# Kernel tuning notes

Measured on AMD Instinct MI355X. Metric: run time of the kernel, lower is better.

Reference implementation:

```python
import jax, jax.numpy as jnp
import numpy as np

B_, S_, D_, N_, R_ = 2, 2048, 1024, 16, 64  # batch, seq, d_model, d_state, dt_rank


def setup_inputs() -> dict:
    key = jax.random.key(0)
    ks = jax.random.split(key, 12)
    x = jax.random.normal(ks[0], (B_, S_, D_), dtype=jnp.float32)
    # params (xavier-ish scale)
    W_dtw = jax.random.normal(ks[1], (R_, D_), dtype=jnp.float32) * (1.0 / np.sqrt(D_))
    W_dt = jax.random.normal(ks[2], (D_, R_), dtype=jnp.float32) * (1.0 / np.sqrt(R_))
    b_dt = jnp.zeros((D_,), dtype=jnp.float32)
    A_log = jnp.log(jax.random.uniform(ks[3], (D_, N_), minval=0.5, maxval=1.5, dtype=jnp.float32))
    W_B = jax.random.normal(ks[4], (N_, D_), dtype=jnp.float32) * (1.0 / np.sqrt(D_))
    W_C = jax.random.normal(ks[5], (N_, D_), dtype=jnp.float32) * (1.0 / np.sqrt(D_))
    Dp = jnp.ones((D_,), dtype=jnp.float32)
    ln_g = jnp.ones((D_,), dtype=jnp.float32)
    ln_b = jnp.zeros((D_,), dtype=jnp.float32)
    W_out = jax.random.normal(ks[6], (D_, D_), dtype=jnp.float32) * (1.0 / np.sqrt(D_))
    return {"x": x, "W_dtw": W_dtw, "W_dt": W_dt, "b_dt": b_dt, "A_log": A_log,
            "W_B": W_B, "W_C": W_C, "Dp": Dp, "ln_g": ln_g, "ln_b": ln_b, "W_out": W_out}


def _layernorm(y, g, b, eps=1e-5):
    mu = jnp.mean(y, axis=-1, keepdims=True)
    var = jnp.mean(jnp.square(y - mu), axis=-1, keepdims=True)
    return (y - mu) * jax.lax.rsqrt(var + eps) * g + b


def reference(x, W_dtw, W_dt, b_dt, A_log, W_B, W_C, Dp, ln_g, ln_b, W_out):
    # projections
    dt = jnp.einsum('bsd,rd->bsr', x, W_dtw)                 # [B,S,R]
    delta = jax.nn.softplus(jnp.einsum('bsr,dr->bsd', dt, W_dt) + b_dt)  # [B,S,D]
    Bm = jnp.einsum('bsd,nd->bsn', x, W_B)                   # [B,S,N]
    Cm = jnp.einsum('bsd,nd->bsn', x, W_C)                   # [B,S,N]
    A = -jnp.exp(A_log)                                      # [D,N]

    def step(h, inp):
        d_t, b_t, c_t, x_t = inp                             # [B,D],[B,N],[B,N],[B,D]
        dA = jnp.exp(d_t[..., None] * A)                     # [B,D,N]
        h = dA * h + (d_t[..., None] * b_t[:, None, :]) * x_t[..., None]
        y_t = jnp.sum(h * c_t[:, None, :], axis=-1)          # [B,D]
        return h, y_t

    h0 = jnp.zeros((x.shape[0], x.shape[2], A.shape[1]), dtype=x.dtype)
    xs = (jnp.swapaxes(delta, 0, 1), jnp.swapaxes(Bm, 0, 1),
          jnp.swapaxes(Cm, 0, 1), jnp.swapaxes(x, 0, 1))
    _, ys = jax.lax.scan(step, h0, xs)                       # ys: [S,B,D]
    y = jnp.swapaxes(ys, 0, 1) + Dp * x                      # [B,S,D]
    y = _layernorm(y, ln_g, ln_b)
    return jnp.einsum('bsd,ed->bse', y, W_out)
```

## Files before the change

kernel.cpp:

```cpp
#include <hip/hip_runtime.h>
#include <hip/hip_bf16.h>

#define B_ 2
#define S_ 2048
#define D_ 1024
#define N_ 16
#define R_ 64
#define NC 64
#define CL 32
#define BS_ (B_*S_)
#define KSPLIT 8

typedef __attribute__((ext_vector_type(4))) float f32x4;
typedef __attribute__((ext_vector_type(8))) short bf16x8;
typedef __attribute__((ext_vector_type(8))) unsigned short u16x8;

__device__ __forceinline__ unsigned short f2b(float v) {
  unsigned u = __builtin_bit_cast(unsigned, v);
  unsigned r = ((u >> 16) & 1u) + 0x7FFFu;
  return (unsigned short)((u + r) >> 16);
}

__device__ __forceinline__ void gload_lds16(const void* g, void* l) {
  __builtin_amdgcn_global_load_lds(
      (const __attribute__((address_space(1))) unsigned int*)g,
      (__attribute__((address_space(3))) unsigned int*)l, 16, 0, 0);
}

__global__ __launch_bounds__(256) void k_castall(
    const float* __restrict__ W_dtw, const float* __restrict__ W_B,
    const float* __restrict__ W_C, const float* __restrict__ W_dt,
    const float* __restrict__ W_out,
    unsigned short* __restrict__ Wcat, unsigned short* __restrict__ wdtb,
    unsigned short* __restrict__ wob) {
  int i = (blockIdx.x * 256 + threadIdx.x) * 4;
  const float* s; unsigned short* d; int off;
  if (i < 65536)       { s = W_dtw; d = Wcat;         off = 0; }
  else if (i < 81920)  { s = W_B;   d = Wcat + 65536; off = 65536; }
  else if (i < 98304)  { s = W_C;   d = Wcat + 81920; off = 81920; }
  else if (i < 163840) { s = W_dt;  d = wdtb;         off = 98304; }
  else                 { s = W_out; d = wob;          off = 163840; }
  int j = i - off;
  float4 v = *(const float4*)&s[j];
  ushort4 o;
  o.x = f2b(v.x); o.y = f2b(v.y); o.z = f2b(v.z); o.w = f2b(v.w);
  *(ushort4*)&d[j] = o;
}

__global__ __launch_bounds__(256, 2) void k_proj(
    const float* __restrict__ x, const unsigned short* __restrict__ Wcat,
    float* __restrict__ part) {
  __shared__ __align__(16) unsigned short Xs[2][64 * 64];
  __shared__ __align__(16) unsigned short Ws[2][96 * 64];
  const int tid = threadIdx.x;
  const int lane = tid & 63, w = tid >> 6;
  const size_t row0 = (size_t)blockIdx.x * 64;
  const int kbase = blockIdx.y * (D_ / KSPLIT);
  f32x4 acc[6] = {};

  auto stage = [&](int buf, int k0) {
    #pragma unroll
    for (int i = 0; i < 2; ++i) {
      int id = i * 256 + tid; int row = id >> 3, s = id & 7;
      const float* gp = &x[(row0 + row) * D_ + k0 + s * 8];
      float4 v0 = *(const float4*)gp;
      float4 v1 = *(const float4*)(gp + 4);
      u16x8 u;
      u[0] = f2b(v0.x); u[1] = f2b(v0.y); u[2] = f2b(v0.z); u[3] = f2b(v0.w);
      u[4] = f2b(v1.x); u[5] = f2b(v1.y); u[6] = f2b(v1.z); u[7] = f2b(v1.w);
      *(u16x8*)&Xs[buf][row * 64 + ((s ^ (row & 7)) << 3)] = u;
    }
    #pragma unroll
    for (int i = 0; i < 3; ++i) {
      int id = i * 256 + tid; int row = id >> 3, s = id & 7;
      gload_lds16(Wcat + (size_t)row * D_ + k0 + ((s ^ (row & 7)) << 3),
                  Ws[buf] + row * 64 + s * 8);
    }
  };
  stage(0, kbase);
  __syncthreads();
  int cur = 0;
  const int r = lane & 15, kg = lane >> 4;
  for (int t = 0; t < 2; ++t) {
    if (t < 1) stage(cur ^ 1, kbase + 64);
    #pragma unroll
    for (int ks = 0; ks < 2; ++ks) {
      const int arow = w * 16 + r;
      bf16x8 a = *(const bf16x8*)&Xs[cur][arow * 64 + ((((ks << 2) | kg) ^ (arow & 7)) << 3)];
      #pragma unroll
      for (int nt = 0; nt < 6; ++nt) {
        const int brow = nt * 16 + r;
        bf16x8 b = *(const bf16x8*)&Ws[cur][brow * 64 + ((((ks << 2) | kg) ^ (brow & 7)) << 3)];
        acc[nt] = __builtin_amdgcn_mfma_f32_16x16x32_bf16(a, b, acc[nt], 0, 0, 0);
      }
    }
    __syncthreads();
    cur ^= 1;
  }
  const int cr = lane >> 4, cc = lane & 15;
  float* pb = part + (size_t)blockIdx.y * (BS_ * 96);
  #pragma unroll
  for (int nt = 0; nt < 6; ++nt)
    #pragma unroll
    for (int j = 0; j < 4; ++j)
      pb[(row0 + w * 16 + cr * 4 + j) * 96 + nt * 16 + cc] = acc[nt][j];
}

__global__ __launch_bounds__(256) void k_projred(
    const float* __restrict__ part, unsigned short* __restrict__ dtb,
    float* __restrict__ Bm, float* __restrict__ Cm) {
  int e = blockIdx.x * 256 + threadIdx.x;
  int row = e / 96, col = e - row * 96;
  float s = 0.f;
  #pragma unroll
  for (int p = 0; p < KSPLIT; ++p) s += part[e + (size_t)p * (BS_ * 96)];
  if (col < 64)      dtb[row * R_ + col] = f2b(s);
  else if (col < 80) Bm[row * N_ + col - 64] = s;
  else               Cm[row * N_ + col - 80] = s;
}

__global__ __launch_bounds__(256) void k_delta(
    const unsigned short* __restrict__ dtb, const unsigned short* __restrict__ wdtb,
    const float* __restrict__ b_dt, float* __restrict__ delta) {
  __shared__ __align__(16) unsigned short As[128 * 64];
  __shared__ __align__(16) unsigned short Bs[128 * 64];
  const int tid = threadIdx.x;
  const int lane = tid & 63, wid = tid >> 6;
  const int wr = wid >> 1, wc = wid & 1;
  const size_t row0 = (size_t)blockIdx.x * 128;
  const size_t col0 = (size_t)blockIdx.y * 128;
  f32x4 acc[4][4] = {};

  {
    const int r = tid >> 3, s = tid & 7;
    #pragma unroll
    for (int i = 0; i < 4; ++i) {
      const int row = i * 32 + r;
      const int gs = s ^ (row & 7);
      gload_lds16(dtb + (row0 + row) * R_ + gs * 8, As + row * 64 + s * 8);
      gload_lds16(wdtb + (col0 + row) * R_ + gs * 8, Bs + row * 64 + s * 8);
    }
  }
  __syncthreads();
  const int r = lane & 15, kg = lane >> 4;
  #pragma unroll
  for (int ks = 0; ks < 2; ++ks) {
    bf16x8 a[4], b[4];
    #pragma unroll
    for (int m = 0; m < 4; ++m) {
      const int arow = wr * 64 + m * 16 + r;
      a[m] = *(const bf16x8*)&As[arow * 64 + (((ks << 2) | kg) ^ (arow & 7)) * 8];
    }
    #pragma unroll
    for (int n = 0; n < 4; ++n) {
      const int brow = wc * 64 + n * 16 + r;
      b[n] = *(const bf16x8*)&Bs[brow * 64 + (((ks << 2) | kg) ^ (brow & 7)) * 8];
    }
    #pragma unroll
    for (int m = 0; m < 4; ++m)
      #pragma unroll
      for (int n = 0; n < 4; ++n)
        acc[m][n] = __builtin_amdgcn_mfma_f32_16x16x32_bf16(a[m], b[n], acc[m][n], 0, 0, 0);
  }
  const int cr = lane >> 4, cc = lane & 15;
  #pragma unroll
  for (int m = 0; m < 4; ++m) {
    #pragma unroll
    for (int n = 0; n < 4; ++n) {
      const int d = (int)col0 + wc * 64 + n * 16 + cc;
      const float bd = b_dt[d];
      #pragma unroll
      for (int j = 0; j < 4; ++j) {
        size_t trow = row0 + wr * 64 + m * 16 + cr * 4 + j;
        float v = acc[m][n][j] + bd;
        float sp = fmaxf(v, 0.f) + log1pf(__expf(-fabsf(v)));
        delta[trow * D_ + d] = sp;
      }
    }
  }
}

__global__ __launch_bounds__(256) void k_scan1(
    const float* __restrict__ x, const float* __restrict__ delta,
    const float* __restrict__ Bm, const float* __restrict__ A_log,
    float* __restrict__ aprod, float* __restrict__ hend) {
  __shared__ __align__(16) float sd[CL][64];
  __shared__ __align__(16) float sx[CL][64];
  __shared__ __align__(16) float sB[CL][N_];
  const int tid = threadIdx.x;
  const int db = blockIdx.x & 15;
  const int c  = (blockIdx.x >> 4) & (NC - 1);
  const int b  = blockIdx.x >> 10;
  const int d0 = db * 64;
  const size_t tokbase = (size_t)(b * S_ + c * CL);

  {
    int s = tid >> 4, jf = (tid & 15) * 4;
    size_t g = (tokbase + s) * D_ + d0 + jf;
    gload_lds16(&delta[g], &sd[s][jf]);
    gload_lds16(&x[g],     &sx[s][jf]);
    gload_lds16(&delta[g + (size_t)16 * D_], &sd[s + 16][jf]);
    gload_lds16(&x[g + (size_t)16 * D_],     &sx[s + 16][jf]);
    if (tid < 128) {
      int s2 = tid >> 2, nf = (tid & 3) * 4;
      gload_lds16(&Bm[(tokbase + s2) * N_ + nf], &sB[s2][nf]);
    }
  }
  const int nq = tid & 3, dl = tid >> 2;
  const int d = d0 + dl;
  float4 av = *(const float4*)&A_log[(size_t)d * N_ + nq * 4];
  float Ad0 = -__expf(av.x), Ad1 = -__expf(av.y);
  float Ad2 = -__expf(av.z), Ad3 = -__expf(av.w);
  __syncthreads();

  float ap0 = 1.f, ap1 = 1.f, ap2 = 1.f, ap3 = 1.f;
  float h0 = 0.f, h1 = 0.f, h2 = 0.f, h3 = 0.f;
  #pragma unroll 8
  for (int s = 0; s < CL; ++s) {
    float dlt = sd[s][dl];
    float dbx = dlt * sx[s][dl];
    float4 Bv = *(const float4*)&sB[s][nq * 4];
    float da0 = __expf(dlt * Ad0), da1 = __expf(dlt * Ad1);
    float da2 = __expf(dlt * Ad2), da3 = __expf(dlt * Ad3);
    ap0 *= da0; ap1 *= da1; ap2 *= da2; ap3 *= da3;
    h0 = da0 * h0 + dbx * Bv.x;
    h1 = da1 * h1 + dbx * Bv.y;
    h2 = da2 * h2 + dbx * Bv.z;
    h3 = da3 * h3 + dbx * Bv.w;
  }
  size_t o = (((size_t)(b * NC + c)) * D_ + d) * N_ + nq * 4;
  *(float4*)&aprod[o] = make_float4(ap0, ap1, ap2, ap3);
  *(float4*)&hend[o]  = make_float4(h0, h1, h2, h3);
}

__global__ __launch_bounds__(256) void k_scan2(
    const float* __restrict__ aprod, const float* __restrict__ hend,
    float* __restrict__ hstart) {
  int g = blockIdx.x * 256 + threadIdx.x;
  int n = g & (N_ - 1);
  int d = (g >> 4) & (D_ - 1);
  int b = g >> 14;
  float h = 0.f;
  for (int c = 0; c < NC; ++c) {
    size_t idx = (((size_t)b * NC + c) * D_ + d) * N_ + n;
    hstart[idx] = h;
    h = aprod[idx] * h + hend[idx];
  }
}

__global__ __launch_bounds__(256) void k_scan3(
    const float* __restrict__ x, const float* __restrict__ delta,
    const float* __restrict__ Bm, const float* __restrict__ Cm,
    const float* __restrict__ A_log, const float* __restrict__ hstart,
    const float* __restrict__ Dp, float* __restrict__ ypre) {
  __shared__ __align__(16) float sd[CL][64];
  __shared__ __align__(16) float sx[CL][64];
  __shared__ __align__(16) float sB[CL][N_];
  __shared__ __align__(16) float sC[CL][N_];
  __shared__ __align__(16) float sy[CL][64];
  const int tid = threadIdx.x;
  const int db = blockIdx.x & 15;
  const int c  = (blockIdx.x >> 4) & (NC - 1);
  const int b  = blockIdx.x >> 10;
  const int d0 = db * 64;
  const size_t tokbase = (size_t)(b * S_ + c * CL);

  {
    int s = tid >> 4, jf = (tid & 15) * 4;
    size_t g = (tokbase + s) * D_ + d0 + jf;
    gload_lds16(&delta[g], &sd[s][jf]);
    gload_lds16(&x[g],     &sx[s][jf]);
    gload_lds16(&delta[g + (size_t)16 * D_], &sd[s + 16][jf]);
    gload_lds16(&x[g + (size_t)16 * D_],     &sx[s + 16][jf]);
    if (tid < 128) {
      int s2 = tid >> 2, nf = (tid & 3) * 4;
      gload_lds16(&Bm[(tokbase + s2) * N_ + nf], &sB[s2][nf]);
      gload_lds16(&Cm[(tokbase + s2) * N_ + nf], &sC[s2][nf]);
    }
  }
  const int nq = tid & 3, dl = tid >> 2;
  const int d = d0 + dl;
  float4 av = *(const float4*)&A_log[(size_t)d * N_ + nq * 4];
  float Ad0 = -__expf(av.x), Ad1 = -__expf(av.y);
  float Ad2 = -__expf(av.z), Ad3 = -__expf(av.w);
  float h0, h1, h2, h3;
  {
    size_t o = (((size_t)(b * NC + c)) * D_ + d) * N_ + nq * 4;
    float4 v = *(const float4*)&hstart[o];
    h0 = v.x; h1 = v.y; h2 = v.z; h3 = v.w;
  }
  const float Dpd = Dp[d];
  __syncthreads();

  #pragma unroll 8
  for (int s = 0; s < CL; ++s) {
    float dlt = sd[s][dl];
    float xv  = sx[s][dl];
    float dbx = dlt * xv;
    float4 Bv = *(const float4*)&sB[s][nq * 4];
    float4 Cv = *(const float4*)&sC[s][nq * 4];
    float da0 = __expf(dlt * Ad0), da1 = __expf(dlt * Ad1);
    float da2 = __expf(dlt * Ad2), da3 = __expf(dlt * Ad3);
    h0 = da0 * h0 + dbx * Bv.x;
    h1 = da1 * h1 + dbx * Bv.y;
    h2 = da2 * h2 + dbx * Bv.z;
    h3 = da3 * h3 + dbx * Bv.w;
    float y = h0 * Cv.x + h1 * Cv.y + h2 * Cv.z + h3 * Cv.w;
    y += __shfl_xor(y, 1);
    y += __shfl_xor(y, 2);
    if (nq == 0) sy[s][dl] = y + Dpd * xv;
  }
  __syncthreads();
  {
    int s = tid >> 3, j = (tid & 7) * 8;
    size_t g = (tokbase + s) * D_ + d0 + j;
    *(float4*)&ypre[g]     = *(float4*)&sy[s][j];
    *(float4*)&ypre[g + 4] = *(float4*)&sy[s][j + 4];
  }
}

__device__ __forceinline__ float block_sum256(float v, float* sm) {
  #pragma unroll
  for (int o = 32; o > 0; o >>= 1) v += __shfl_down(v, o, 64);
  int w = threadIdx.x >> 6;
  __syncthreads();
  if ((threadIdx.x & 63) == 0) sm[w] = v;
  __syncthreads();
  return (sm[0] + sm[1]) + (sm[2] + sm[3]);
}

__global__ __launch_bounds__(256) void k_ln(
    const float* __restrict__ ypre, const float* __restrict__ g,
    const float* __restrict__ bta, unsigned short* __restrict__ ybf) {
  __shared__ float sm[4];
  const int t = blockIdx.x;
  const int tid = threadIdx.x;
  size_t base = (size_t)t * D_ + tid * 4;
  float4 v = *(const float4*)&ypre[base];
  float s1 = block_sum256(v.x + v.y + v.z + v.w, sm);
  float mu = s1 * (1.f / D_);
  float cx = v.x - mu, cy = v.y - mu, cz = v.z - mu, cw = v.w - mu;
  float s2 = block_sum256(cx*cx + cy*cy + cz*cz + cw*cw, sm);
  float rs = rsqrtf(s2 * (1.f / D_) + 1e-5f);
  float4 gg = *(const float4*)&g[tid * 4];
  float4 bb = *(const float4*)&bta[tid * 4];
  ushort4 o;
  o.x = f2b(cx * rs * gg.x + bb.x);
  o.y = f2b(cy * rs * gg.y + bb.y);
  o.z = f2b(cz * rs * gg.z + bb.z);
  o.w = f2b(cw * rs * gg.w + bb.w);
  *(ushort4*)&ybf[base] = o;
}

__device__ __forceinline__ void stage128x64(const unsigned short* __restrict__ g,
                                            size_t row0, int k0,
                                            unsigned short* lds, int tid) {
  const int r = tid >> 3, s = tid & 7;
  #pragma unroll
  for (int i = 0; i < 4; ++i) {
    const int row = i * 32 + r;
    const int gs = s ^ (row & 7);
    gload_lds16(g + ((row0 + row) << 10) + k0 + (gs << 3), lds + row * 64 + s * 8);
  }
}

__device__ __forceinline__ void stage64x64(const unsigned short* __restrict__ g,
                                           size_t row0, int k0,
                                           unsigned short* lds, int tid) {
  const int r = tid >> 3, s = tid & 7;
  #pragma unroll
  for (int i = 0; i < 2; ++i) {
    const int row = i * 32 + r;
    const int gs = s ^ (row & 7);
    gload_lds16(g + ((row0 + row) << 10) + k0 + (gs << 3), lds + row * 64 + s * 8);
  }
}

__global__ __launch_bounds__(256, 2) void k_out(const unsigned short* __restrict__ Y,
                                                const unsigned short* __restrict__ W,
                                                float* __restrict__ O) {
  __shared__ __align__(16) unsigned short As[2][128 * 64];
  __shared__ __align__(16) unsigned short Bs[2][64 * 64];
  const int tid = threadIdx.x;
  const int lane = tid & 63, wid = tid >> 6;
  const size_t row0 = (size_t)blockIdx.x * 128;
  const size_t col0 = (size_t)blockIdx.y * 64;
  f32x4 acc[2][4] = {};

  stage128x64(Y, row0, 0, As[0], tid);
  stage64x64(W, col0, 0, Bs[0], tid);
  __syncthreads();

  int cur = 0;
  const int r = lane & 15, kg = lane >> 4;
  for (int t = 0; t < 16; ++t) {
    if (t + 1 < 16) {
      stage128x64(Y, row0, (t + 1) * 64, As[cur ^ 1], tid);
      stage64x64(W, col0, (t + 1) * 64, Bs[cur ^ 1], tid);
    }
    #pragma unroll
    for (int ks = 0; ks < 2; ++ks) {
      bf16x8 a[2], b[4];
      #pragma unroll
      for (int m = 0; m < 2; ++m) {
        const int arow = wid * 32 + m * 16 + r;
        a[m] = *(const bf16x8*)&As[cur][arow * 64 + (((ks << 2) | kg) ^ (arow & 7)) * 8];
      }
      #pragma unroll
      for (int n = 0; n < 4; ++n) {
        const int brow = n * 16 + r;
        b[n] = *(const bf16x8*)&Bs[cur][brow * 64 + (((ks << 2) | kg) ^ (brow & 7)) * 8];
      }
      #pragma unroll
      for (int m = 0; m < 2; ++m)
        #pragma unroll
        for (int n = 0; n < 4; ++n)
          acc[m][n] = __builtin_amdgcn_mfma_f32_16x16x32_bf16(a[m], b[n], acc[m][n], 0, 0, 0);
    }
    __syncthreads();
    cur ^= 1;
  }

  const int cr = lane >> 4, cc = lane & 15;
  #pragma unroll
  for (int m = 0; m < 2; ++m) {
    #pragma unroll
    for (int n = 0; n < 4; ++n) {
      size_t orow = row0 + wid * 32 + m * 16 + cr * 4;
      float* op = O + orow * D_ + col0 + n * 16 + cc;
      #pragma unroll
      for (int j = 0; j < 4; ++j) op[(size_t)j * D_] = acc[m][n][j];
    }
  }
}

extern "C" void kernel_launch(void* const* d_in, const int* in_sizes, int n_in,
                              void* d_out, int out_size, void* d_ws, size_t ws_size,
                              hipStream_t stream) {
  const float* x     = (const float*)d_in[0];
  const float* W_dtw = (const float*)d_in[1];
  const float* W_dt  = (const float*)d_in[2];
  const float* b_dt  = (const float*)d_in[3];
  const float* A_log = (const float*)d_in[4];
  const float* W_B   = (const float*)d_in[5];
  const float* W_C   = (const float*)d_in[6];
  const float* Dp    = (const float*)d_in[7];
  const float* ln_g  = (const float*)d_in[8];
  const float* ln_b  = (const float*)d_in[9];
  const float* W_out = (const float*)d_in[10];
  float* out = (float*)d_out;

  float* ws = (float*)d_ws;
  float* delta  = ws;
  float* ypre   = delta  + (size_t)BS_ * D_;
  float* Bm     = ypre   + (size_t)BS_ * D_;
  float* Cm     = Bm     + (size_t)BS_ * N_;
  float* aprod  = Cm     + (size_t)BS_ * N_;
  float* hend   = aprod  + (size_t)B_ * NC * D_ * N_;
  float* hstart = hend   + (size_t)B_ * NC * D_ * N_;
  float* part   = hstart + (size_t)B_ * NC * D_ * N_;
  unsigned short* Wcat = (unsigned short*)(part + (size_t)KSPLIT * BS_ * 96);
  unsigned short* wdtb = Wcat + (size_t)96 * D_;
  unsigned short* wob  = wdtb + (size_t)D_ * R_;
  unsigned short* ybf  = wob  + (size_t)D_ * D_;
  unsigned short* dtb  = ybf  + (size_t)BS_ * D_;

  k_castall<<<dim3(1184), dim3(256), 0, stream>>>(W_dtw, W_B, W_C, W_dt, W_out,
                                                  Wcat, wdtb, wob);
  k_proj<<<dim3(BS_ / 64, KSPLIT), dim3(256), 0, stream>>>(x, Wcat, part);
  k_projred<<<dim3(BS_ * 96 / 256), dim3(256), 0, stream>>>(part, dtb, Bm, Cm);
  k_delta<<<dim3(BS_ / 128, D_ / 128), dim3(256), 0, stream>>>(dtb, wdtb, b_dt, delta);
  k_scan1<<<dim3(B_ * NC * (D_ / 64)), dim3(256), 0, stream>>>(x, delta, Bm, A_log,
                                                               aprod, hend);
  k_scan2<<<dim3(B_ * D_ * N_ / 256), dim3(256), 0, stream>>>(aprod, hend, hstart);
  k_scan3<<<dim3(B_ * NC * (D_ / 64)), dim3(256), 0, stream>>>(x, delta, Bm, Cm,
                                                               A_log, hstart, Dp, ypre);
  k_ln<<<dim3(BS_), dim3(256), 0, stream>>>(ypre, ln_g, ln_b, ybf);
  k_out<<<dim3(BS_ / 128, D_ / 64), dim3(256), 0, stream>>>(ybf, wob, out);
}
```

Baseline: 110.6 us.

## Replace per-state chunk decay products with delta sums and parallelize inter-chunk scan

The chunk scan now stores one per-channel sum of delta instead of a per-state product of decays, and the inter-chunk pass rebuilds each decay as exp(A*sum). The second pass splits the 64 chunks across 8 lanes, combining them with a shuffle-based prefix, so the sequential chain drops from 64 dependent steps to about 23. Separately, the output GEMM tile shrinks from 128x64 to 64x64 with higher occupancy, giving more blocks at the cost of less data reuse per block.

```diff
diff --git a/kernel.cpp b/kernel.cpp
--- a/kernel.cpp
+++ b/kernel.cpp
@@ -183,7 +183,7 @@
 __global__ __launch_bounds__(256) void k_scan1(
     const float* __restrict__ x, const float* __restrict__ delta,
     const float* __restrict__ Bm, const float* __restrict__ A_log,
-    float* __restrict__ aprod, float* __restrict__ hend) {
+    float* __restrict__ sdsum, float* __restrict__ hend) {
   __shared__ __align__(16) float sd[CL][64];
   __shared__ __align__(16) float sx[CL][64];
   __shared__ __align__(16) float sB[CL][N_];
@@ -213,38 +213,63 @@
   float Ad2 = -__expf(av.z), Ad3 = -__expf(av.w);
   __syncthreads();
 
-  float ap0 = 1.f, ap1 = 1.f, ap2 = 1.f, ap3 = 1.f;
+  float sds = 0.f;
   float h0 = 0.f, h1 = 0.f, h2 = 0.f, h3 = 0.f;
   #pragma unroll 8
   for (int s = 0; s < CL; ++s) {
     float dlt = sd[s][dl];
     float dbx = dlt * sx[s][dl];
+    sds += dlt;
     float4 Bv = *(const float4*)&sB[s][nq * 4];
     float da0 = __expf(dlt * Ad0), da1 = __expf(dlt * Ad1);
     float da2 = __expf(dlt * Ad2), da3 = __expf(dlt * Ad3);
-    ap0 *= da0; ap1 *= da1; ap2 *= da2; ap3 *= da3;
     h0 = da0 * h0 + dbx * Bv.x;
     h1 = da1 * h1 + dbx * Bv.y;
     h2 = da2 * h2 + dbx * Bv.z;
     h3 = da3 * h3 + dbx * Bv.w;
   }
   size_t o = (((size_t)(b * NC + c)) * D_ + d) * N_ + nq * 4;
-  *(float4*)&aprod[o] = make_float4(ap0, ap1, ap2, ap3);
-  *(float4*)&hend[o]  = make_float4(h0, h1, h2, h3);
+  *(float4*)&hend[o] = make_float4(h0, h1, h2, h3);
+  if (nq == 0) sdsum[(size_t)(b * NC + c) * D_ + d] = sds;
 }
 
 __global__ __launch_bounds__(256) void k_scan2(
-    const float* __restrict__ aprod, const float* __restrict__ hend,
-    float* __restrict__ hstart) {
-  int g = blockIdx.x * 256 + threadIdx.x;
-  int n = g & (N_ - 1);
-  int d = (g >> 4) & (D_ - 1);
-  int b = g >> 14;
+    const float* __restrict__ sdsum, const float* __restrict__ hend,
+    const float* __restrict__ A_log, float* __restrict__ hstart) {
+  const int tid = threadIdx.x;
+  const int o  = tid & 7;
+  const int n  = (tid >> 3) & 15;
+  const int dl = tid >> 7;
+  const int d2 = blockIdx.x & 511;
+  const int b  = blockIdx.x >> 9;
+  const int d  = d2 * 2 + dl;
+  const float Ad = -__expf(A_log[(size_t)d * N_ + n]);
+
+  float ap8[8], he8[8];
+  float A_loc = 1.f, H_loc = 0.f;
+  #pragma unroll
+  for (int k = 0; k < 8; ++k) {
+    const int c = o * 8 + k;
+    float sds = sdsum[(size_t)(b * NC + c) * D_ + d];
+    float ap = __expf(Ad * sds);
+    float he = hend[((size_t)(b * NC + c) * D_ + d) * N_ + n];
+    ap8[k] = ap; he8[k] = he;
+    A_loc *= ap;
+    H_loc = ap * H_loc + he;
+  }
   float h = 0.f;
-  for (int c = 0; c < NC; ++c) {
-    size_t idx = (((size_t)b * NC + c) * D_ + d) * N_ + n;
-    hstart[idx] = h;
-    h = aprod[idx] * h + hend[idx];
+  const int gb = (tid & 63) & ~7;
+  #pragma unroll
+  for (int j = 0; j < 7; ++j) {
+    float Aj = __shfl(A_loc, gb | j, 64);
+    float Hj = __shfl(H_loc, gb | j, 64);
+    if (o > j) h = Aj * h + Hj;
+  }
+  #pragma unroll
+  for (int k = 0; k < 8; ++k) {
+    const int c = o * 8 + k;
+    hstart[((size_t)(b * NC + c) * D_ + d) * N_ + n] = h;
+    h = ap8[k] * h + he8[k];
   }
 }
 
@@ -352,18 +377,6 @@
   *(ushort4*)&ybf[base] = o;
 }
 
-__device__ __forceinline__ void stage128x64(const unsigned short* __restrict__ g,
-                                            size_t row0, int k0,
-                                            unsigned short* lds, int tid) {
-  const int r = tid >> 3, s = tid & 7;
-  #pragma unroll
-  for (int i = 0; i < 4; ++i) {
-    const int row = i * 32 + r;
-    const int gs = s ^ (row & 7);
-    gload_lds16(g + ((row0 + row) << 10) + k0 + (gs << 3), lds + row * 64 + s * 8);
-  }
-}
-
 __device__ __forceinline__ void stage64x64(const unsigned short* __restrict__ g,
                                            size_t row0, int k0,
                                            unsigned short* lds, int tid) {
@@ -376,18 +389,18 @@
   }
 }
 
-__global__ __launch_bounds__(256, 2) void k_out(const unsigned short* __restrict__ Y,
+__global__ __launch_bounds__(256, 4) void k_out(const unsigned short* __restrict__ Y,
                                                 const unsigned short* __restrict__ W,
                                                 float* __restrict__ O) {
-  __shared__ __align__(16) unsigned short As[2][128 * 64];
+  __shared__ __align__(16) unsigned short As[2][64 * 64];
   __shared__ __align__(16) unsigned short Bs[2][64 * 64];
   const int tid = threadIdx.x;
   const int lane = tid & 63, wid = tid >> 6;
-  const size_t row0 = (size_t)blockIdx.x * 128;
+  const size_t row0 = (size_t)blockIdx.x * 64;
   const size_t col0 = (size_t)blockIdx.y * 64;
-  f32x4 acc[2][4] = {};
-
-  stage128x64(Y, row0, 0, As[0], tid);
+  f32x4 acc[4] = {};
+
+  stage64x64(Y, row0, 0, As[0], tid);
   stage64x64(W, col0, 0, Bs[0], tid);
   __syncthreads();
 
@@ -395,27 +408,22 @@
   const int r = lane & 15, kg = lane >> 4;
   for (int t = 0; t < 16; ++t) {
     if (t + 1 < 16) {
-      stage128x64(Y, row0, (t + 1) * 64, As[cur ^ 1], tid);
+      stage64x64(Y, row0, (t + 1) * 64, As[cur ^ 1], tid);
       stage64x64(W, col0, (t + 1) * 64, Bs[cur ^ 1], tid);
     }
     #pragma unroll
     for (int ks = 0; ks < 2; ++ks) {
-      bf16x8 a[2], b[4];
-      #pragma unroll
-      for (int m = 0; m < 2; ++m) {
-        const int arow = wid * 32 + m * 16 + r;
-        a[m] = *(const bf16x8*)&As[cur][arow * 64 + (((ks << 2) | kg) ^ (arow & 7)) * 8];
-      }
-      #pragma unroll
-      for (int n = 0; n < 4; ++n) {
-        const int brow = n * 16 + r;
-        b[n] = *(const bf16x8*)&Bs[cur][brow * 64 + (((ks << 2) | kg) ^ (brow & 7)) * 8];
-      }
-      #pragma unroll
-      for (int m = 0; m < 2; ++m)
-        #pragma unroll
-        for (int n = 0; n < 4; ++n)
-          acc[m][n] = __builtin_amdgcn_mfma_f32_16x16x32_bf16(a[m], b[n], acc[m][n], 0, 0, 0);
+      const int arow = wid * 16 + r;
+      bf16x8 a = *(const bf16x8*)&As[cur][arow * 64 + (((ks << 2) | kg) ^ (arow & 7)) * 8];
+      bf16x8 b0, b1, b2, b3;
+      b0 = *(const bf16x8*)&Bs[cur][(0 * 16 + r) * 64 + (((ks << 2) | kg) ^ ((0 * 16 + r) & 7)) * 8];
+      b1 = *(const bf16x8*)&Bs[cur][(1 * 16 + r) * 64 + (((ks << 2) | kg) ^ ((1 * 16 + r) & 7)) * 8];
+      b2 = *(const bf16x8*)&Bs[cur][(2 * 16 + r) * 64 + (((ks << 2) | kg) ^ ((2 * 16 + r) & 7)) * 8];
+      b3 = *(const bf16x8*)&Bs[cur][(3 * 16 + r) * 64 + (((ks << 2) | kg) ^ ((3 * 16 + r) & 7)) * 8];
+      acc[0] = __builtin_amdgcn_mfma_f32_16x16x32_bf16(a, b0, acc[0], 0, 0, 0);
+      acc[1] = __builtin_amdgcn_mfma_f32_16x16x32_bf16(a, b1, acc[1], 0, 0, 0);
+      acc[2] = __builtin_amdgcn_mfma_f32_16x16x32_bf16(a, b2, acc[2], 0, 0, 0);
+      acc[3] = __builtin_amdgcn_mfma_f32_16x16x32_bf16(a, b3, acc[3], 0, 0, 0);
     }
     __syncthreads();
     cur ^= 1;
@@ -423,14 +431,11 @@
 
   const int cr = lane >> 4, cc = lane & 15;
   #pragma unroll
-  for (int m = 0; m < 2; ++m) {
-    #pragma unroll
-    for (int n = 0; n < 4; ++n) {
-      size_t orow = row0 + wid * 32 + m * 16 + cr * 4;
-      float* op = O + orow * D_ + col0 + n * 16 + cc;
-      #pragma unroll
-      for (int j = 0; j < 4; ++j) op[(size_t)j * D_] = acc[m][n][j];
-    }
+  for (int n = 0; n < 4; ++n) {
+    size_t orow = row0 + wid * 16 + cr * 4;
+    float* op = O + orow * D_ + col0 + n * 16 + cc;
+    #pragma unroll
+    for (int j = 0; j < 4; ++j) op[(size_t)j * D_] = acc[n][j];
   }
 }
 
@@ -455,10 +460,10 @@
   float* ypre   = delta  + (size_t)BS_ * D_;
   float* Bm     = ypre   + (size_t)BS_ * D_;
   float* Cm     = Bm     + (size_t)BS_ * N_;
-  float* aprod  = Cm     + (size_t)BS_ * N_;
-  float* hend   = aprod  + (size_t)B_ * NC * D_ * N_;
+  float* hend   = Cm     + (size_t)BS_ * N_;
   float* hstart = hend   + (size_t)B_ * NC * D_ * N_;
-  float* part   = hstart + (size_t)B_ * NC * D_ * N_;
+  float* sdsum  = hstart + (size_t)B_ * NC * D_ * N_;
+  float* part   = sdsum  + (size_t)B_ * NC * D_;
   unsigned short* Wcat = (unsigned short*)(part + (size_t)KSPLIT * BS_ * 96);
   unsigned short* wdtb = Wcat + (size_t)96 * D_;
   unsigned short* wob  = wdtb + (size_t)D_ * R_;
@@ -471,10 +476,10 @@
   k_projred<<<dim3(BS_ * 96 / 256), dim3(256), 0, stream>>>(part, dtb, Bm, Cm);
   k_delta<<<dim3(BS_ / 128, D_ / 128), dim3(256), 0, stream>>>(dtb, wdtb, b_dt, delta);
   k_scan1<<<dim3(B_ * NC * (D_ / 64)), dim3(256), 0, stream>>>(x, delta, Bm, A_log,
-                                                               aprod, hend);
-  k_scan2<<<dim3(B_ * D_ * N_ / 256), dim3(256), 0, stream>>>(aprod, hend, hstart);
+                                                               sdsum, hend);
+  k_scan2<<<dim3(B_ * (D_ / 2)), dim3(256), 0, stream>>>(sdsum, hend, A_log, hstart);
   k_scan3<<<dim3(B_ * NC * (D_ / 64)), dim3(256), 0, stream>>>(x, delta, Bm, Cm,
                                                                A_log, hstart, Dp, ypre);
   k_ln<<<dim3(BS_), dim3(256), 0, stream>>>(ypre, ln_g, ln_b, ybf);
-  k_out<<<dim3(BS_ / 128, D_ / 64), dim3(256), 0, stream>>>(ybf, wob, out);
-}
+  k_out<<<dim3(BS_ / 64, D_ / 64), dim3(256), 0, stream>>>(ybf, wob, out);
+}
```

After: 111.9 us. Within noise of the previous version (+1.2%).
